# Performance work log

Hardware: AMD Instinct MI355X
Metric: run time of the kernel (lower is better)

## Reference

```python
import jax, jax.numpy as jnp
import numpy as np

EPS_LN = 1e-5
EPS_D = 1e-8
K = 3

def layer_norm(x, g, b):
    mu = jnp.mean(x, axis=-1, keepdims=True)
    var = jnp.var(x, axis=-1, keepdims=True)
    return (x - mu) * jax.lax.rsqrt(var + EPS_LN) * g + b

def setup_inputs() -> dict:
    key = jax.random.key(0)
    ks = jax.random.split(key, 8)
    Nc, Nu, Cin, Cout = 4096, 16384, 256, 256
    return {
        "x_feat": jax.random.normal(ks[0], (Nc, Cin), jnp.float32),
        "x_pos": jax.random.uniform(ks[1], (Nc, 3), jnp.float32),
        "xup_feat": jax.random.normal(ks[2], (Nu, Cout), jnp.float32),
        "xup_pos": jax.random.uniform(ks[3], (Nu, 3), jnp.float32),
        "g1": jnp.ones((Cin,), jnp.float32),
        "b1": jnp.zeros((Cin,), jnp.float32),
        "W": jax.random.normal(ks[4], (Cin, Cout), jnp.float32) * 0.02,
        "b": jnp.zeros((Cout,), jnp.float32),
        "g2": jnp.ones((Cout,), jnp.float32),
        "b2": jnp.zeros((Cout,), jnp.float32),
        "W_up": jax.random.normal(ks[5], (Cout, Cout), jnp.float32) * 0.02,
        "b_up": jnp.zeros((Cout,), jnp.float32),
    }

def reference(x_feat, x_pos, xup_feat, xup_pos, g1, b1, W, b, g2, b2, W_up, b_up):
    # norm -> linear on coarse points: [Nc, Cout]
    x = layer_norm(x_feat, g1, b1) @ W + b
    # norm -> linear on fine points:   [Nu, Cout]
    xu = layer_norm(xup_feat, g2, b2) @ W_up + b_up
    # squared pairwise distances fine->coarse: [Nu, Nc]
    d2 = (jnp.sum(xup_pos * xup_pos, axis=-1, keepdims=True)
          - 2.0 * (xup_pos @ x_pos.T)
          + jnp.sum(x_pos * x_pos, axis=-1))
    # k nearest coarse neighbors per fine point
    neg_d2, idx = jax.lax.top_k(-d2, K)          # [Nu, K]
    w = 1.0 / (-neg_d2 + EPS_D)                  # inverse-distance weights
    w = w / jnp.sum(w, axis=-1, keepdims=True)
    # gather + weighted sum: [Nu, Cout]
    interp = jnp.einsum('uk,ukc->uc', w, x[idx])
    return interp + xu
```

## Files before the change

### kernel.cpp

```cpp
#include <hip/hip_runtime.h>

#define EPS_LN 1e-5f
#define EPS_D  1e-8f
#define BIGD 3.402823466e+38f

typedef __attribute__((ext_vector_type(8))) short s16x8;
typedef __attribute__((ext_vector_type(4))) float f32x4;
typedef __attribute__((ext_vector_type(4))) unsigned short u16x4;

#define XC_OFF    0u
#define XH_OFF    4194304u
#define XL_OFF    14680064u
#define MU_OFF    25165824u
#define RS_OFF    25247744u
#define WGH_OFF   25329664u
#define WGL_OFF   25460736u
#define WUGH_OFF  25591808u
#define WUGL_OFF  25722880u
#define C12_OFF   25853952u
#define CPS_OFF   25858048u
#define IDXS_OFF  25923584u
#define CST_OFF   25939968u

__device__ __forceinline__ int cell_of(float px, float py, float pz) {
    int cx = (int)(px * 8.0f); cx = cx < 0 ? 0 : (cx > 7 ? 7 : cx);
    int cy = (int)(py * 8.0f); cy = cy < 0 ? 0 : (cy > 7 ? 7 : cy);
    int cz = (int)(pz * 8.0f); cz = cz < 0 ? 0 : (cz > 7 ? 7 : cz);
    return (cz * 8 + cy) * 8 + cx;
}

__global__ __launch_bounds__(256) void prep_kernel(
    const float* __restrict__ x_feat, const float* __restrict__ xup_feat,
    const float* __restrict__ x_pos,
    const float* __restrict__ W, const float* __restrict__ W_up,
    const float* __restrict__ g1, const float* __restrict__ b1,
    const float* __restrict__ g2, const float* __restrict__ b2,
    float* __restrict__ mu, float* __restrict__ rs,
    unsigned short* __restrict__ xh, unsigned short* __restrict__ xl,
    unsigned short* __restrict__ wgh, unsigned short* __restrict__ wgl,
    unsigned short* __restrict__ wugh, unsigned short* __restrict__ wugl,
    float* __restrict__ c12,
    float4* __restrict__ cps, int* __restrict__ idxs, int* __restrict__ cellStart)
{
    __shared__ int cnt[512];
    __shared__ int ofs[512];
    __shared__ int wpart[4];

    const int bid = blockIdx.x, tid = threadIdx.x;
    const int lane = tid & 63, wave = tid >> 6;

    if (bid < 640) {
        #pragma unroll
        for (int rr = 0; rr < 8; ++rr) {
            const int r = bid * 32 + wave * 8 + rr;
            const float* src = (r < 16384) ? (xup_feat + (size_t)r * 256)
                                           : (x_feat + (size_t)(r - 16384) * 256);
            const float4 v = ((const float4*)src)[lane];
            float s  = v.x + v.y + v.z + v.w;
            float ss = v.x*v.x + v.y*v.y + v.z*v.z + v.w*v.w;
            #pragma unroll
            for (int off = 1; off < 64; off <<= 1) {
                s  += __shfl_xor(s,  off);
                ss += __shfl_xor(ss, off);
            }
            if (lane == 0) {
                const float m   = s * (1.0f / 256.0f);
                const float var = ss * (1.0f / 256.0f) - m * m;
                mu[r] = m;
                rs[r] = rsqrtf(var + EPS_LN);
            }
            const float vv[4] = { v.x, v.y, v.z, v.w };
            u16x4 hv, lv;
            #pragma unroll
            for (int c = 0; c < 4; ++c) {
                const unsigned ua = __float_as_uint(vv[c]);
                hv[c] = (unsigned short)(ua >> 16);
                const float lo = vv[c] - __uint_as_float(ua & 0xFFFF0000u);
                lv[c] = (unsigned short)(__float_as_uint(lo) >> 16);
            }
            *(u16x4*)&xh[(size_t)r * 256 + lane * 4] = hv;
            *(u16x4*)&xl[(size_t)r * 256 + lane * 4] = lv;
        }
    } else if (bid < 656) {
        const int mb = bid - 640;
        const float* src = (mb < 8) ? W : W_up;
        const float* g   = (mb < 8) ? g1 : g2;
        unsigned short* dh = (mb < 8) ? wgh : wugh;
        unsigned short* dl = (mb < 8) ? wgl : wugl;
        const int n  = (mb & 7) * 32 + (tid >> 3);
        const int kc = (tid & 7) * 32;
        for (int kk = 0; kk < 32; kk += 4) {
            u16x4 hv, lv;
            #pragma unroll
            for (int c = 0; c < 4; ++c) {
                const int k = kc + kk + c;
                const float wv = g[k] * src[(size_t)k * 256 + n];
                const unsigned ua = __float_as_uint(wv);
                hv[c] = (unsigned short)(ua >> 16);
                const float lo = wv - __uint_as_float(ua & 0xFFFF0000u);
                lv[c] = (unsigned short)(__float_as_uint(lo) >> 16);
            }
            *(u16x4*)&dh[(size_t)n * 256 + kc + kk] = hv;
            *(u16x4*)&dl[(size_t)n * 256 + kc + kk] = lv;
        }
    } else if (bid < 658) {
        const bool fine = (bid == 657);
        const float* src = fine ? W_up : W;
        const float* g   = fine ? g2 : g1;
        const float* bln = fine ? b2 : b1;
        float* c1 = c12 + (fine ? 0 : 512);
        float* c2 = c12 + (fine ? 256 : 768);
        float a1 = 0.0f, a2 = 0.0f;
        for (int k = 0; k < 256; ++k) {
            const float wv = src[(size_t)k * 256 + tid];
            a1 = fmaf(bln[k], wv, a1);
            a2 = fmaf(g[k],   wv, a2);
        }
        c1[tid] = a1;
        c2[tid] = a2;
    } else {
        cnt[tid] = 0; cnt[tid + 256] = 0;
        __syncthreads();
        for (int i = tid; i < 4096; i += 256) {
            const int c = cell_of(x_pos[i*3+0], x_pos[i*3+1], x_pos[i*3+2]);
            atomicAdd(&cnt[c], 1);
        }
        __syncthreads();
        const int base = wave * 128 + lane * 2;
        const int a = cnt[base], b = cnt[base + 1];
        const int p = a + b;
        int incl = p;
        #pragma unroll
        for (int off = 1; off < 64; off <<= 1) {
            const int t = __shfl_up(incl, off);
            if (lane >= off) incl += t;
        }
        if (lane == 63) wpart[wave] = incl;
        __syncthreads();
        int woff = 0;
        for (int w = 0; w < 4; ++w) if (w < wave) woff += wpart[w];
        const int e0 = woff + (incl - p);
        ofs[base] = e0;          ofs[base + 1] = e0 + a;
        cellStart[base] = e0;    cellStart[base + 1] = e0 + a;
        if (tid == 0) cellStart[512] = 4096;
        __syncthreads();
        for (int i = tid; i < 4096; i += 256) {
            const float px = x_pos[i*3+0], py = x_pos[i*3+1], pz = x_pos[i*3+2];
            const int c = cell_of(px, py, pz);
            const int pos = atomicAdd(&ofs[c], 1);
            cps[pos] = make_float4(px, py, pz, px*px + py*py + pz*pz);
            idxs[pos] = i;
        }
    }
}

__global__ __launch_bounds__(256) void gemm_kernel(
    const unsigned short* __restrict__ xh, const unsigned short* __restrict__ xl,
    const float* __restrict__ mu, const float* __restrict__ rs,
    const unsigned short* __restrict__ wgh, const unsigned short* __restrict__ wgl,
    const unsigned short* __restrict__ wugh, const unsigned short* __restrict__ wugl,
    const float* __restrict__ c12,
    const float* __restrict__ b_up, const float* __restrict__ bb,
    float* __restrict__ outF, float* __restrict__ outC)
{
    const int bid = blockIdx.x;
    const unsigned short *BH, *BL; const float *c1, *c2, *bias; float* OUT;
    int row0, col0, statbase;
    if (bid < 256) {
        BH = wugh; BL = wugl; c1 = c12; c2 = c12 + 256; bias = b_up; OUT = outF;
        row0 = (bid >> 1) * 128; col0 = (bid & 1) * 128; statbase = 0;
    } else {
        const int id = bid - 256;
        BH = wgh; BL = wgl; c1 = c12 + 512; c2 = c12 + 768; bias = bb; OUT = outC;
        row0 = (id >> 1) * 128; col0 = (id & 1) * 128; statbase = 16384;
    }

    const int lane = threadIdx.x & 63;
    const int wave = threadIdx.x >> 6;
    const int wr = wave >> 1, wc = wave & 1;
    const int lm = lane & 15, lk = lane >> 4;

    int arow[4];
    #pragma unroll
    for (int mf = 0; mf < 4; ++mf)
        arow[mf] = statbase + row0 + wr * 64 + mf * 16 + lm;

    int ncol[4]; float c1v[4], c2v[4], bv[4];
    #pragma unroll
    for (int nf = 0; nf < 4; ++nf) {
        ncol[nf] = col0 + wc * 64 + nf * 16 + lm;
        c1v[nf] = c1[ncol[nf]];
        c2v[nf] = c2[ncol[nf]];
        bv[nf]  = bias[ncol[nf]];
    }

    f32x4 acc[4][4];
    #pragma unroll
    for (int mf = 0; mf < 4; ++mf)
        #pragma unroll
        for (int nf = 0; nf < 4; ++nf)
            acc[mf][nf] = (f32x4){0.0f, 0.0f, 0.0f, 0.0f};

    for (int k0 = 0; k0 < 256; k0 += 32) {
        const int kb = k0 + lk * 8;

        s16x8 bh[4], bl[4], ah[4], al[4];
        #pragma unroll
        for (int nf = 0; nf < 4; ++nf) {
            const size_t o = (size_t)ncol[nf] * 256 + kb;
            bh[nf] = *(const s16x8*)(BH + o);
            bl[nf] = *(const s16x8*)(BL + o);
        }
        #pragma unroll
        for (int mf = 0; mf < 4; ++mf) {
            const size_t o = (size_t)arow[mf] * 256 + kb;
            ah[mf] = *(const s16x8*)(xh + o);
            al[mf] = *(const s16x8*)(xl + o);
        }

        #pragma unroll
        for (int mf = 0; mf < 4; ++mf)
            #pragma unroll
            for (int nf = 0; nf < 4; ++nf) {
                acc[mf][nf] = __builtin_amdgcn_mfma_f32_16x16x32_bf16(ah[mf], bh[nf], acc[mf][nf], 0, 0, 0);
                acc[mf][nf] = __builtin_amdgcn_mfma_f32_16x16x32_bf16(ah[mf], bl[nf], acc[mf][nf], 0, 0, 0);
                acc[mf][nf] = __builtin_amdgcn_mfma_f32_16x16x32_bf16(al[mf], bh[nf], acc[mf][nf], 0, 0, 0);
            }
    }

    #pragma unroll
    for (int mf = 0; mf < 4; ++mf) {
        #pragma unroll
        for (int q = 0; q < 4; ++q) {
            const int orow = row0 + wr * 64 + mf * 16 + lk * 4 + q;
            const float m = mu[statbase + orow];
            const float s = rs[statbase + orow];
            const float ms = -m * s;
            #pragma unroll
            for (int nf = 0; nf < 4; ++nf)
                OUT[(size_t)orow * 256 + ncol[nf]] =
                    fmaf(s, acc[mf][nf][q], fmaf(ms, c2v[nf], c1v[nf]) + bv[nf]);
        }
    }
}

__device__ __forceinline__ void ins3(float d, int p,
    float& b0, float& b1, float& b2, int& p0, int& p1, int& p2)
{
    const bool lt0 = d < b0, lt1 = d < b1, lt2 = d < b2;
    const float n1 = lt0 ? b0 : (lt1 ? d : b1);
    const int   q1 = lt0 ? p0 : (lt1 ? p : p1);
    const float n2 = lt1 ? b1 : (lt2 ? d : b2);
    const int   q2 = lt1 ? p1 : (lt2 ? p : p2);
    b0 = lt0 ? d : b0;  p0 = lt0 ? p : p0;
    b1 = n1; p1 = q1;
    b2 = n2; p2 = q2;
}

__global__ __launch_bounds__(512) void topk_kernel(
    const float4* __restrict__ cps, const int* __restrict__ idxs,
    const int* __restrict__ cellStart,
    const float* __restrict__ xup_pos,
    const float* __restrict__ xc, float* __restrict__ out)
{
    __shared__ float pd[8][64][3];
    __shared__ int   pp[8][64][3];
    __shared__ float wsel[64][3];
    __shared__ int   isel[64][3];
    __shared__ int   cst[513];

    const int tid = threadIdx.x, lane = tid & 63, wave = tid >> 6;
    const int u = blockIdx.x * 64 + lane;

    for (int i = tid; i < 513; i += 512) cst[i] = cellStart[i];

    const float ux = xup_pos[u * 3 + 0];
    const float uy = xup_pos[u * 3 + 1];
    const float uz = xup_pos[u * 3 + 2];
    const float uu = ux * ux + uy * uy + uz * uz;
    int cx = (int)(ux * 8.0f); cx = cx < 0 ? 0 : (cx > 7 ? 7 : cx);
    int cy = (int)(uy * 8.0f); cy = cy < 0 ? 0 : (cy > 7 ? 7 : cy);
    int cz = (int)(uz * 8.0f); cz = cz < 0 ? 0 : (cz > 7 ? 7 : cz);

    __syncthreads();

    float b0 = BIGD, b1 = BIGD, b2 = BIGD;
    int p0 = 0, p1 = 0, p2 = 0;

    for (int cc = wave; cc < 27; cc += 8) {
        const int nx = cx + (cc % 3) - 1;
        const int ny = cy + ((cc / 3) % 3) - 1;
        const int nz = cz + (cc / 9) - 1;
        if ((unsigned)nx > 7u || (unsigned)ny > 7u || (unsigned)nz > 7u) continue;
        const int cell = (nz * 8 + ny) * 8 + nx;
        const int s = cst[cell], e = cst[cell + 1];
        if (s >= e) continue;
        float4 c = cps[s];
        for (int p = s; p < e; ++p) {
            const float4 nxt = (p + 1 < e) ? cps[p + 1] : c;
            const float dot = ux * c.x + uy * c.y + uz * c.z;
            const float d = (uu - 2.0f * dot) + c.w;
            ins3(d, p, b0, b1, b2, p0, p1, p2);
            c = nxt;
        }
    }

    pd[wave][lane][0] = b0; pd[wave][lane][1] = b1; pd[wave][lane][2] = b2;
    pp[wave][lane][0] = p0; pp[wave][lane][1] = p1; pp[wave][lane][2] = p2;
    __syncthreads();

    if (wave == 0) {
        for (int w = 1; w < 8; ++w) {
            #pragma unroll
            for (int e = 0; e < 3; ++e)
                ins3(pd[w][lane][e], pp[w][lane][e], b0, b1, b2, p0, p1, p2);
        }

        const float h = 0.125f;
        float gmin = BIGD;
        if (cx > 0) gmin = fminf(gmin, ux - (float)(cx - 1) * h);
        if (cx < 7) gmin = fminf(gmin, (float)(cx + 2) * h - ux);
        if (cy > 0) gmin = fminf(gmin, uy - (float)(cy - 1) * h);
        if (cy < 7) gmin = fminf(gmin, (float)(cy + 2) * h - uy);
        if (cz > 0) gmin = fminf(gmin, uz - (float)(cz - 1) * h);
        if (cz < 7) gmin = fminf(gmin, (float)(cz + 2) * h - uz);

        if (b2 > gmin * gmin) {
            b0 = b1 = b2 = BIGD; p0 = p1 = p2 = 0;
            for (int p = 0; p < 4096; ++p) {
                const float4 c = cps[p];
                const float dot = ux * c.x + uy * c.y + uz * c.z;
                const float d = (uu - 2.0f * dot) + c.w;
                ins3(d, p, b0, b1, b2, p0, p1, p2);
            }
        }

        float w0 = 1.0f / (b0 + EPS_D);
        float w1 = 1.0f / (b1 + EPS_D);
        float w2 = 1.0f / (b2 + EPS_D);
        const float inv = 1.0f / (w0 + w1 + w2);
        wsel[lane][0] = w0 * inv; wsel[lane][1] = w1 * inv; wsel[lane][2] = w2 * inv;
        isel[lane][0] = idxs[p0]; isel[lane][1] = idxs[p1]; isel[lane][2] = idxs[p2];
    }
    __syncthreads();

    #pragma unroll
    for (int r = 0; r < 8; ++r) {
        const int ul = wave * 8 + r;
        const float w0 = wsel[ul][0], w1 = wsel[ul][1], w2 = wsel[ul][2];
        const int a0 = isel[ul][0], a1 = isel[ul][1], a2 = isel[ul][2];
        const float4 v0 = ((const float4*)(xc + (size_t)a0 * 256))[lane];
        const float4 v1 = ((const float4*)(xc + (size_t)a1 * 256))[lane];
        const float4 v2 = ((const float4*)(xc + (size_t)a2 * 256))[lane];
        float4* op = (float4*)(out + (size_t)(blockIdx.x * 64 + ul) * 256);
        float4 o = op[lane];
        o.x += w0 * v0.x + w1 * v1.x + w2 * v2.x;
        o.y += w0 * v0.y + w1 * v1.y + w2 * v2.y;
        o.z += w0 * v0.z + w1 * v1.z + w2 * v2.z;
        o.w += w0 * v0.w + w1 * v1.w + w2 * v2.w;
        op[lane] = o;
    }
}

extern "C" void kernel_launch(void* const* d_in, const int* in_sizes, int n_in,
                              void* d_out, int out_size, void* d_ws, size_t ws_size,
                              hipStream_t stream)
{
    const float* x_feat   = (const float*)d_in[0];
    const float* x_pos    = (const float*)d_in[1];
    const float* xup_feat = (const float*)d_in[2];
    const float* xup_pos  = (const float*)d_in[3];
    const float* g1       = (const float*)d_in[4];
    const float* b1       = (const float*)d_in[5];
    const float* W        = (const float*)d_in[6];
    const float* bb       = (const float*)d_in[7];
    const float* g2       = (const float*)d_in[8];
    const float* b2       = (const float*)d_in[9];
    const float* W_up     = (const float*)d_in[10];
    const float* b_up     = (const float*)d_in[11];

    float* out = (float*)d_out;
    char*  ws  = (char*)d_ws;

    float* xc  = (float*)(ws + XC_OFF);
    unsigned short* xh   = (unsigned short*)(ws + XH_OFF);
    unsigned short* xl   = (unsigned short*)(ws + XL_OFF);
    float* mu  = (float*)(ws + MU_OFF);
    float* rs  = (float*)(ws + RS_OFF);
    unsigned short* wgh  = (unsigned short*)(ws + WGH_OFF);
    unsigned short* wgl  = (unsigned short*)(ws + WGL_OFF);
    unsigned short* wugh = (unsigned short*)(ws + WUGH_OFF);
    unsigned short* wugl = (unsigned short*)(ws + WUGL_OFF);
    float* c12 = (float*)(ws + C12_OFF);
    float4* cps = (float4*)(ws + CPS_OFF);
    int* idxs   = (int*)(ws + IDXS_OFF);
    int* cstart = (int*)(ws + CST_OFF);

    prep_kernel<<<659, 256, 0, stream>>>(x_feat, xup_feat, x_pos, W, W_up,
                                         g1, b1, g2, b2,
                                         mu, rs, xh, xl,
                                         wgh, wgl, wugh, wugl,
                                         c12, cps, idxs, cstart);
    gemm_kernel<<<320, 256, 0, stream>>>(xh, xl, mu, rs,
                                         wgh, wgl, wugh, wugl,
                                         c12, b_up, bb, out, xc);
    topk_kernel<<<256, 512, 0, stream>>>(cps, idxs, cstart, xup_pos, xc, out);
}
```

Baseline: 167.3 us.

## Sort fine points by spatial cell so top-k blocks share neighbor cells

Adds a second binning block in the prep kernel that counting-sorts the 16384 fine points into the same 8x8x8 grid. The top-k kernel then processes fine points in cell order, so each wave's lanes scan mostly the same neighbor cells with little divergence, and results are scattered back through the stored permutation. The top-k block shrinks from 8 to 4 waves, each covering more neighbor cells and 16 output rows in the gather phase. The extra cost is a single-block serial sort of 16384 points on the critical path and non-contiguous output writes.

```diff
diff --git a/kernel.cpp b/kernel.cpp
--- a/kernel.cpp
+++ b/kernel.cpp
@@ -21,6 +21,8 @@
 #define CPS_OFF   25858048u
 #define IDXS_OFF  25923584u
 #define CST_OFF   25939968u
+#define UPS_OFF   25944064u
+#define USORT_OFF 26206208u
 
 __device__ __forceinline__ int cell_of(float px, float py, float pz) {
     int cx = (int)(px * 8.0f); cx = cx < 0 ? 0 : (cx > 7 ? 7 : cx);
@@ -31,7 +33,7 @@
 
 __global__ __launch_bounds__(256) void prep_kernel(
     const float* __restrict__ x_feat, const float* __restrict__ xup_feat,
-    const float* __restrict__ x_pos,
+    const float* __restrict__ x_pos, const float* __restrict__ xup_pos,
     const float* __restrict__ W, const float* __restrict__ W_up,
     const float* __restrict__ g1, const float* __restrict__ b1,
     const float* __restrict__ g2, const float* __restrict__ b2,
@@ -40,7 +42,8 @@
     unsigned short* __restrict__ wgh, unsigned short* __restrict__ wgl,
     unsigned short* __restrict__ wugh, unsigned short* __restrict__ wugl,
     float* __restrict__ c12,
-    float4* __restrict__ cps, int* __restrict__ idxs, int* __restrict__ cellStart)
+    float4* __restrict__ cps, int* __restrict__ idxs, int* __restrict__ cellStart,
+    float4* __restrict__ ups, int* __restrict__ usort)
 {
     __shared__ int cnt[512];
     __shared__ int ofs[512];
@@ -119,10 +122,14 @@
         c1[tid] = a1;
         c2[tid] = a2;
     } else {
+        const bool fine = (bid == 659);
+        const int npts = fine ? 16384 : 4096;
+        const float* pos = fine ? xup_pos : x_pos;
+
         cnt[tid] = 0; cnt[tid + 256] = 0;
         __syncthreads();
-        for (int i = tid; i < 4096; i += 256) {
-            const int c = cell_of(x_pos[i*3+0], x_pos[i*3+1], x_pos[i*3+2]);
+        for (int i = tid; i < npts; i += 256) {
+            const int c = cell_of(pos[i*3+0], pos[i*3+1], pos[i*3+2]);
             atomicAdd(&cnt[c], 1);
         }
         __syncthreads();
@@ -141,15 +148,22 @@
         for (int w = 0; w < 4; ++w) if (w < wave) woff += wpart[w];
         const int e0 = woff + (incl - p);
         ofs[base] = e0;          ofs[base + 1] = e0 + a;
-        cellStart[base] = e0;    cellStart[base + 1] = e0 + a;
-        if (tid == 0) cellStart[512] = 4096;
+        if (!fine) {
+            cellStart[base] = e0;    cellStart[base + 1] = e0 + a;
+            if (tid == 0) cellStart[512] = 4096;
+        }
         __syncthreads();
-        for (int i = tid; i < 4096; i += 256) {
-            const float px = x_pos[i*3+0], py = x_pos[i*3+1], pz = x_pos[i*3+2];
+        for (int i = tid; i < npts; i += 256) {
+            const float px = pos[i*3+0], py = pos[i*3+1], pz = pos[i*3+2];
             const int c = cell_of(px, py, pz);
-            const int pos = atomicAdd(&ofs[c], 1);
-            cps[pos] = make_float4(px, py, pz, px*px + py*py + pz*pz);
-            idxs[pos] = i;
+            const int slot = atomicAdd(&ofs[c], 1);
+            if (fine) {
+                ups[slot] = make_float4(px, py, pz, px*px + py*py + pz*pz);
+                usort[slot] = i;
+            } else {
+                cps[slot] = make_float4(px, py, pz, px*px + py*py + pz*pz);
+                idxs[slot] = i;
+            }
         }
     }
 }
@@ -257,27 +271,27 @@
     b2 = n2; p2 = q2;
 }
 
-__global__ __launch_bounds__(512) void topk_kernel(
+__global__ __launch_bounds__(256) void topk_kernel(
     const float4* __restrict__ cps, const int* __restrict__ idxs,
     const int* __restrict__ cellStart,
-    const float* __restrict__ xup_pos,
+    const float4* __restrict__ ups, const int* __restrict__ usort,
     const float* __restrict__ xc, float* __restrict__ out)
 {
-    __shared__ float pd[8][64][3];
-    __shared__ int   pp[8][64][3];
+    __shared__ float pd[4][64][3];
+    __shared__ int   pp[4][64][3];
     __shared__ float wsel[64][3];
     __shared__ int   isel[64][3];
+    __shared__ int   uor[64];
     __shared__ int   cst[513];
 
     const int tid = threadIdx.x, lane = tid & 63, wave = tid >> 6;
-    const int u = blockIdx.x * 64 + lane;
-
-    for (int i = tid; i < 513; i += 512) cst[i] = cellStart[i];
-
-    const float ux = xup_pos[u * 3 + 0];
-    const float uy = xup_pos[u * 3 + 1];
-    const float uz = xup_pos[u * 3 + 2];
-    const float uu = ux * ux + uy * uy + uz * uz;
+    const int su = blockIdx.x * 64 + lane;
+
+    for (int i = tid; i < 513; i += 256) cst[i] = cellStart[i];
+
+    const float4 up = ups[su];
+    const float ux = up.x, uy = up.y, uz = up.z, uu = up.w;
+    if (wave == 0) uor[lane] = usort[su];
     int cx = (int)(ux * 8.0f); cx = cx < 0 ? 0 : (cx > 7 ? 7 : cx);
     int cy = (int)(uy * 8.0f); cy = cy < 0 ? 0 : (cy > 7 ? 7 : cy);
     int cz = (int)(uz * 8.0f); cz = cz < 0 ? 0 : (cz > 7 ? 7 : cz);
@@ -287,7 +301,7 @@
     float b0 = BIGD, b1 = BIGD, b2 = BIGD;
     int p0 = 0, p1 = 0, p2 = 0;
 
-    for (int cc = wave; cc < 27; cc += 8) {
+    for (int cc = wave; cc < 27; cc += 4) {
         const int nx = cx + (cc % 3) - 1;
         const int ny = cy + ((cc / 3) % 3) - 1;
         const int nz = cz + (cc / 9) - 1;
@@ -310,7 +324,7 @@
     __syncthreads();
 
     if (wave == 0) {
-        for (int w = 1; w < 8; ++w) {
+        for (int w = 1; w < 4; ++w) {
             #pragma unroll
             for (int e = 0; e < 3; ++e)
                 ins3(pd[w][lane][e], pp[w][lane][e], b0, b1, b2, p0, p1, p2);
@@ -345,14 +359,14 @@
     __syncthreads();
 
     #pragma unroll
-    for (int r = 0; r < 8; ++r) {
-        const int ul = wave * 8 + r;
+    for (int r = 0; r < 16; ++r) {
+        const int ul = wave * 16 + r;
         const float w0 = wsel[ul][0], w1 = wsel[ul][1], w2 = wsel[ul][2];
         const int a0 = isel[ul][0], a1 = isel[ul][1], a2 = isel[ul][2];
         const float4 v0 = ((const float4*)(xc + (size_t)a0 * 256))[lane];
         const float4 v1 = ((const float4*)(xc + (size_t)a1 * 256))[lane];
         const float4 v2 = ((const float4*)(xc + (size_t)a2 * 256))[lane];
-        float4* op = (float4*)(out + (size_t)(blockIdx.x * 64 + ul) * 256);
+        float4* op = (float4*)(out + (size_t)uor[ul] * 256);
         float4 o = op[lane];
         o.x += w0 * v0.x + w1 * v1.x + w2 * v2.x;
         o.y += w0 * v0.y + w1 * v1.y + w2 * v2.y;
@@ -395,14 +409,16 @@
     float4* cps = (float4*)(ws + CPS_OFF);
     int* idxs   = (int*)(ws + IDXS_OFF);
     int* cstart = (int*)(ws + CST_OFF);
-
-    prep_kernel<<<659, 256, 0, stream>>>(x_feat, xup_feat, x_pos, W, W_up,
-                                         g1, b1, g2, b2,
+    float4* ups = (float4*)(ws + UPS_OFF);
+    int* usort  = (int*)(ws + USORT_OFF);
+
+    prep_kernel<<<660, 256, 0, stream>>>(x_feat, xup_feat, x_pos, xup_pos,
+                                         W, W_up, g1, b1, g2, b2,
                                          mu, rs, xh, xl,
                                          wgh, wgl, wugh, wugl,
-                                         c12, cps, idxs, cstart);
+                                         c12, cps, idxs, cstart, ups, usort);
     gemm_kernel<<<320, 256, 0, stream>>>(xh, xl, mu, rs,
                                          wgh, wgl, wugh, wugl,
                                          c12, b_up, bb, out, xc);
-    topk_kernel<<<256, 512, 0, stream>>>(cps, idxs, cstart, xup_pos, xc, out);
-}
+    topk_kernel<<<256, 256, 0, stream>>>(cps, idxs, cstart, ups, usort, xc, out);
+}
```

Result: slower. 192.4 us (+15.0%).
